# Kernel optimization log

Hardware: AMD Instinct MI355X
Metric: run time of the kernel (lower is better)

## Reference

```python
import jax, jax.numpy as jnp
import numpy as np

B, D, L, TABLE, C, HID = 32768, 8, 16, 524288, 2, 512
GROWTH = 1.3
_PRIMES = [2654436881, 5915587277, 1500450271, 3267000013, 5754853343, 4093082899, 9576890767, 3628273133]
# torch mixes int64/int32 with python-int scalars; only the low 32 bits matter for
# mod-by-power-of-two table_size, so int32 wraparound arithmetic is bit-exact here.
PRIMES32 = jnp.asarray(np.array([p % (1 << 32) for p in _PRIMES], dtype=np.uint64).astype(np.uint32).view(np.int32))


def _linear_init(key, out_f, in_f):
    s = 1.0 / np.sqrt(in_f)
    kw, kb = jax.random.split(key)
    w = jax.random.uniform(kw, (out_f, in_f), jnp.float32, -s, s)
    b = jax.random.uniform(kb, (out_f,), jnp.float32, -s, s)
    return w, b


def setup_inputs() -> dict:
    key = jax.random.key(0)
    ks = jax.random.split(key, 6)
    x = jax.random.normal(ks[0], (B, D), jnp.float32)
    T = jax.random.normal(ks[1], (L, TABLE, C), jnp.float32)
    K = jnp.power(jnp.float32(GROWTH), jnp.arange(L, dtype=jnp.float32))[:, None]  # [L,1]
    l1_w, l1_b = _linear_init(ks[2], HID, D + L * C)
    l2_w, l2_b = _linear_init(ks[3], HID, HID)
    act_w, act_b = _linear_init(ks[4], 4, HID)
    val_w, val_b = _linear_init(ks[5], 1, HID)
    return dict(x=x, T=T, K=K, l1_w=l1_w, l1_b=l1_b, l2_w=l2_w, l2_b=l2_b,
                act_w=act_w, act_b=act_b, val_w=val_w, val_b=val_b)


def reference(x, T, K, l1_w, l1_b, l2_w, l2_b, act_w, act_b, val_w, val_b):
    Bn, Dn = x.shape
    Ln, table_size, Cn = T.shape
    p = jnp.cumsum(x, -1)[:, None, :] * K                      # [B,L,D]
    frac = p - jnp.trunc(p)                                    # torch.frac semantics (sign of p)
    c = jnp.sort(frac, -1)                                     # [B,L,D]
    R = (frac[..., None] >= c[..., None, :]).astype(x.dtype)   # [B,L,D,D]
    R = jnp.concatenate([R, jnp.zeros(R.shape[:-1] + (1,), x.dtype)], -1)  # [B,L,D,D+1]
    c = jnp.concatenate([c, jnp.ones(c.shape[:-1] + (1,), x.dtype)], -1)   # [B,L,D+1]
    A = R + jnp.floor(p)[..., None]                            # [B,L,D,D+1]
    A = A - jnp.concatenate([jnp.zeros_like(A[..., :1, :]), A[..., :-1, :]], -2)
    c = c - jnp.concatenate([jnp.zeros_like(c[..., :1]), c[..., :-1]], -1)
    Ai = A.astype(jnp.int32)                                   # trunc toward zero, like .int()
    terms = Ai * PRIMES32[None, None, :Dn, None]               # int32 wraparound multiply
    cidx = terms[:, :, 0]
    for i in range(1, Dn):                                     # small fixed D, XOR chain
        cidx = jnp.bitwise_xor(cidx, terms[:, :, i])           # [B,L,D+1]
    idx = jnp.mod(cidx, table_size)                            # floor-mod -> non-negative
    f = T[jnp.arange(Ln)[None, :, None], idx]                  # gather -> [B,L,D+1,C]
    f = (f * c[..., None] / K[:, :, None]).sum(2)              # [B,L,C]
    h = jnp.concatenate([x, f.reshape(Bn, -1)], -1)            # [B, D + L*C]
    h = jax.nn.relu(h @ l1_w.T + l1_b)
    h = jax.nn.relu(h @ l2_w.T + l2_b)
    action = h @ act_w.T + act_b                               # [B,4]
    value = h @ val_w.T + val_b                                # [B,1]
    return action, value
```

## Files before the change

### kernel.cpp

```cpp
#include <hip/hip_runtime.h>
#include <cstdint>
#include <cstddef>

#define BB   32768
#define DD   8
#define LLV  16
#define TBL  524288
#define HID  512

typedef __attribute__((ext_vector_type(8))) short short8;
typedef __attribute__((ext_vector_type(8))) unsigned short u16x8;
typedef __attribute__((ext_vector_type(4))) float f32x4;
typedef __attribute__((ext_vector_type(2))) float f32x2;

__device__ __constant__ uint32_t PR[8] = {
    2654436881u, 1620619981u, 1500450271u, 3267000013u,
    1459886047u, 4093082899u,  986956175u, 3628273133u
};

__device__ __forceinline__ unsigned short f2bf(float f) {
    uint32_t u = __float_as_uint(f);
    uint32_t r = (u + 0x7fffu + ((u >> 16) & 1u)) >> 16;
    return (unsigned short)r;
}

__device__ __forceinline__ void gload_lds16(const void* gsrc, void* ldst) {
    __builtin_amdgcn_global_load_lds(
        (const __attribute__((address_space(1))) unsigned int*)gsrc,
        (__attribute__((address_space(3))) unsigned int*)ldst,
        16, 0, 0);
}

__device__ __forceinline__ void enc_idx(const float xs[8], float Kl,
                                        uint32_t idx9[9], float w9[9])
{
    float fr[8];
    int   base[8];
    float cs = 0.f;
#pragma unroll
    for (int i2 = 0; i2 < 8; i2++) {
        cs += xs[i2];
        float p = cs * Kl;
        fr[i2]   = p - truncf(p);
        base[i2] = (int)floorf(p);
    }

    float c[8];
#pragma unroll
    for (int i2 = 0; i2 < 8; i2++) c[i2] = fr[i2];
#define CE(a_, b_) { float lo_ = fminf(c[a_], c[b_]); float hi_ = fmaxf(c[a_], c[b_]); c[a_] = lo_; c[b_] = hi_; }
    CE(0,1) CE(2,3) CE(4,5) CE(6,7)
    CE(0,2) CE(1,3) CE(4,6) CE(5,7)
    CE(1,2) CE(5,6) CE(0,4) CE(3,7)
    CE(1,5) CE(2,6)
    CE(1,4) CE(3,6)
    CE(2,4) CE(3,5)
    CE(3,4)
#undef CE

    float prevc = 0.f;
#pragma unroll
    for (int j = 0; j < 9; j++) {
        float cj = (j < 8) ? c[j] : 1.0f;
        uint32_t h = 0;
        int prev = 0;
#pragma unroll
        for (int i2 = 0; i2 < 8; i2++) {
            int ai = base[i2] + (fr[i2] >= cj ? 1 : 0);
            h ^= (uint32_t)(ai - prev) * PR[i2];
            prev = ai;
        }
        idx9[j] = h & (TBL - 1);
        w9[j]   = cj - prevc;
        prevc   = cj;
    }
}

__global__ __launch_bounds__(256) void k_encode(
    const float* __restrict__ x, const float* __restrict__ T,
    const float* __restrict__ Karr, unsigned short* __restrict__ h0T)
{
    int i = blockIdx.x;
    int l = (i & 7) + ((i >> 10) << 3);
    int b = ((i & 1023) >> 3) * 256 + threadIdx.x;

    const float4 x0 = *(const float4*)(x + (size_t)b * DD);
    const float4 x1 = *(const float4*)(x + (size_t)b * DD + 4);
    float xs[8] = {x0.x, x0.y, x0.z, x0.w, x1.x, x1.y, x1.z, x1.w};

    float Kl = Karr[l];
    const f32x2* Tl = (const f32x2*)(T + ((size_t)l * TBL) * 2);

    uint32_t idx9[9];
    float    w9[9];
    enc_idx(xs, Kl, idx9, w9);

    f32x2 t0, t1, t2, t3, t4, t5, t6, t7, t8;
#define GL(n) asm volatile("global_load_dwordx2 %0, %1, off" \
                           : "=v"(t##n) : "v"(Tl + idx9[n]));
    GL(0) GL(1) GL(2) GL(3) GL(4) GL(5) GL(6) GL(7) GL(8)
#undef GL
    asm volatile("s_waitcnt vmcnt(0)"
        : "+v"(t0), "+v"(t1), "+v"(t2), "+v"(t3), "+v"(t4),
          "+v"(t5), "+v"(t6), "+v"(t7), "+v"(t8));
    __builtin_amdgcn_sched_barrier(0);

    float f0, f1;
    f0 = t0[0] * w9[0];  f1 = t0[1] * w9[0];
    f0 = fmaf(t1[0], w9[1], f0); f1 = fmaf(t1[1], w9[1], f1);
    f0 = fmaf(t2[0], w9[2], f0); f1 = fmaf(t2[1], w9[2], f1);
    f0 = fmaf(t3[0], w9[3], f0); f1 = fmaf(t3[1], w9[3], f1);
    f0 = fmaf(t4[0], w9[4], f0); f1 = fmaf(t4[1], w9[4], f1);
    f0 = fmaf(t5[0], w9[5], f0); f1 = fmaf(t5[1], w9[5], f1);
    f0 = fmaf(t6[0], w9[6], f0); f1 = fmaf(t6[1], w9[6], f1);
    f0 = fmaf(t7[0], w9[7], f0); f1 = fmaf(t7[1], w9[7], f1);
    f0 = fmaf(t8[0], w9[8], f0); f1 = fmaf(t8[1], w9[8], f1);
    f0 /= Kl;
    f1 /= Kl;

    h0T[(size_t)(l * 2 + 0) * BB + b] = f2bf(f0);
    h0T[(size_t)(l * 2 + 1) * BB + b] = f2bf(f1);
}

__global__ __launch_bounds__(256) void k_pack(
    const unsigned short* __restrict__ h0T, const float* __restrict__ x,
    unsigned short* __restrict__ h0b)
{
    int b = blockIdx.x * 256 + threadIdx.x;
    unsigned short row[64];
    const float4 x0 = *(const float4*)(x + (size_t)b * 8);
    const float4 x1 = *(const float4*)(x + (size_t)b * 8 + 4);
    row[0] = f2bf(x0.x); row[1] = f2bf(x0.y); row[2] = f2bf(x0.z); row[3] = f2bf(x0.w);
    row[4] = f2bf(x1.x); row[5] = f2bf(x1.y); row[6] = f2bf(x1.z); row[7] = f2bf(x1.w);
#pragma unroll
    for (int p = 0; p < 32; p++) row[8 + p] = h0T[(size_t)p * BB + b];
#pragma unroll
    for (int c = 40; c < 64; c++) row[c] = 0;
#pragma unroll
    for (int i = 0; i < 8; i++)
        *(u16x8*)(h0b + (size_t)b * 64 + i * 8) = *(u16x8*)(row + i * 8);
}

__global__ __launch_bounds__(256) void k_cvtw(
    const float* __restrict__ w2, unsigned short* __restrict__ w2p,
    const float* __restrict__ w1, unsigned short* __restrict__ w1p)
{
    int bid = blockIdx.x;
    if (bid < 128) {
        int u  = bid * 256 + threadIdx.x;
        int kg = u & 3, kc = (u >> 2) & 15, c = u >> 6;
        const float* src = w2 + (size_t)c * 512 + kc * 32 + kg * 8;
        unsigned short fr[8];
#pragma unroll
        for (int e = 0; e < 8; ++e) fr[e] = f2bf(src[e]);
        *(u16x8*)(w2p + ((((size_t)kc * 512 + c) * 4 + kg) << 3)) = *(u16x8*)fr;
    } else {
        int u  = (bid - 128) * 256 + threadIdx.x;
        int kg = u & 3, ks = (u >> 2) & 1, c = u >> 3;
        int kbase = ks * 32 + kg * 8;
        unsigned short fr[8];
#pragma unroll
        for (int e = 0; e < 8; ++e) {
            int k = kbase + e;
            fr[e] = (k < 40) ? f2bf(w1[(size_t)c * 40 + k]) : (unsigned short)0;
        }
        *(u16x8*)(w1p + ((((size_t)ks * 512 + c) * 4 + kg) << 3)) = *(u16x8*)fr;
    }
}

__global__ __launch_bounds__(512, 2) void k_fused(
    const unsigned short* __restrict__ h0b, const unsigned short* __restrict__ w1p,
    const unsigned short* __restrict__ w2p, const float* __restrict__ b1,
    const float* __restrict__ b2, const float* __restrict__ aw,
    const float* __restrict__ vw, float* __restrict__ hpart)
{
    __shared__ unsigned short h1s[128 * 512];
    __shared__ unsigned short h0s[128 * 64];

    const int tid  = threadIdx.x;
    const int wid  = tid >> 6;
    const int lane = tid & 63;
    const int wm = wid >> 2, wn = wid & 3;
    const int lr = lane & 15;
    const int kg = lane >> 4;
    const int b0 = blockIdx.x * 128;

#pragma unroll
    for (int it = 0; it < 2; ++it) {
        int offb  = (it * 512 + tid) << 4;
        int loffb = offb ^ (((offb >> 7) & 7) << 4);
        int row = loffb >> 7;
        int kel = (loffb & 127) >> 1;
        int ldsbyte = ((it * 512) + (wid * 64)) << 4;
        gload_lds16(h0b + (size_t)(b0 + row) * 64 + kel, (char*)h0s + ldsbyte);
    }
    __syncthreads();

    f32x4 acc[4][8];
#pragma unroll
    for (int m = 0; m < 4; ++m)
#pragma unroll
        for (int n = 0; n < 8; ++n) acc[m][n] = (f32x4){0.f, 0.f, 0.f, 0.f};

#pragma unroll
    for (int ks = 0; ks < 2; ++ks) {
        int kbyte = ks * 64 + kg * 16;
        short8 af[4];
#pragma unroll
        for (int m = 0; m < 4; ++m) {
            int row = wm * 64 + m * 16 + lr;
            int a = ((row << 7) + kbyte) ^ ((row & 7) << 4);
            af[m] = *(const short8*)((const char*)h0s + a);
        }
        short8 bfr[8];
#pragma unroll
        for (int n = 0; n < 8; ++n) {
            int col = wn * 128 + n * 16 + lr;
            bfr[n] = *(const short8*)(w1p + ((((size_t)ks * 512 + col) * 4 + kg) << 3));
        }
#pragma unroll
        for (int m = 0; m < 4; ++m)
#pragma unroll
            for (int n = 0; n < 8; ++n)
                acc[m][n] = __builtin_amdgcn_mfma_f32_16x16x32_bf16(
                    af[m], bfr[n], acc[m][n], 0, 0, 0);
    }

#pragma unroll
    for (int n = 0; n < 8; ++n) {
        int col = wn * 128 + n * 16 + lr;
        float b1v = b1[col];
#pragma unroll
        for (int m = 0; m < 4; ++m) {
#pragma unroll
            for (int r = 0; r < 4; ++r) {
                int row = wm * 64 + m * 16 + kg * 4 + r;
                int byte = ((row << 10) + col * 2) ^ ((row & 7) << 4);
                *(unsigned short*)((char*)h1s + byte) =
                    f2bf(fmaxf(acc[m][n][r] + b1v, 0.f));
            }
        }
    }
    __syncthreads();

#pragma unroll
    for (int m = 0; m < 4; ++m)
#pragma unroll
        for (int n = 0; n < 8; ++n) acc[m][n] = (f32x4){0.f, 0.f, 0.f, 0.f};

    short8 aX[4], bX[8], aY[4], bY[8];

#define LDA(dst, kc)                                                            \
    _Pragma("unroll")                                                           \
    for (int m = 0; m < 4; ++m) {                                               \
        int row = wm * 64 + m * 16 + lr;                                        \
        int a = (((row << 10) + (kc) * 64 + kg * 16)) ^ ((row & 7) << 4);       \
        dst[m] = *(const short8*)((const char*)h1s + a);                        \
    }
#define LDB(dst, kc)                                                            \
    _Pragma("unroll")                                                           \
    for (int n = 0; n < 8; ++n) {                                               \
        int col = wn * 128 + n * 16 + lr;                                       \
        dst[n] = *(const short8*)(w2p + ((((size_t)(kc) * 512 + col) * 4 + kg) << 3)); \
    }
#define MM(aa, bb)                                                              \
    __builtin_amdgcn_sched_barrier(0);                                          \
    __builtin_amdgcn_s_setprio(1);                                              \
    _Pragma("unroll")                                                           \
    for (int m = 0; m < 4; ++m)                                                 \
        _Pragma("unroll")                                                       \
        for (int n = 0; n < 8; ++n)                                             \
            acc[m][n] = __builtin_amdgcn_mfma_f32_16x16x32_bf16(                \
                aa[m], bb[n], acc[m][n], 0, 0, 0);                              \
    __builtin_amdgcn_s_setprio(0);

    LDA(aX, 0)  LDB(bX, 0)
    LDA(aY, 1)  LDB(bY, 1)  MM(aX, bX)
    LDA(aX, 2)  LDB(bX, 2)  MM(aY, bY)
    LDA(aY, 3)  LDB(bY, 3)  MM(aX, bX)
    LDA(aX, 4)  LDB(bX, 4)  MM(aY, bY)
    LDA(aY, 5)  LDB(bY, 5)  MM(aX, bX)
    LDA(aX, 6)  LDB(bX, 6)  MM(aY, bY)
    LDA(aY, 7)  LDB(bY, 7)  MM(aX, bX)
    LDA(aX, 8)  LDB(bX, 8)  MM(aY, bY)
    LDA(aY, 9)  LDB(bY, 9)  MM(aX, bX)
    LDA(aX, 10) LDB(bX, 10) MM(aY, bY)
    LDA(aY, 11) LDB(bY, 11) MM(aX, bX)
    LDA(aX, 12) LDB(bX, 12) MM(aY, bY)
    LDA(aY, 13) LDB(bY, 13) MM(aX, bX)
    LDA(aX, 14) LDB(bX, 14) MM(aY, bY)
    LDA(aY, 15) LDB(bY, 15) MM(aX, bX)
    MM(aY, bY)
#undef LDA
#undef LDB
#undef MM

#pragma unroll
    for (int n = 0; n < 8; ++n) {
        int col = wn * 128 + n * 16 + lr;
        float b2v = b2[col];
#pragma unroll
        for (int m = 0; m < 4; ++m)
#pragma unroll
            for (int r = 0; r < 4; ++r)
                acc[m][n][r] = fmaxf(acc[m][n][r] + b2v, 0.f);
    }

    float hwv[5][8];
#pragma unroll
    for (int n = 0; n < 8; ++n) {
        int col = wn * 128 + n * 16 + lr;
        hwv[0][n] = aw[col];
        hwv[1][n] = aw[512 + col];
        hwv[2][n] = aw[1024 + col];
        hwv[3][n] = aw[1536 + col];
        hwv[4][n] = vw[col];
    }
    float* hp = hpart + (size_t)wn * (BB * 5);
#pragma unroll
    for (int hm = 0; hm < 5; ++hm) {
        f32x4 p[4];
#pragma unroll
        for (int m = 0; m < 4; ++m) {
            p[m] = acc[m][0] * hwv[hm][0];
#pragma unroll
            for (int n = 1; n < 8; ++n) p[m] += acc[m][n] * hwv[hm][n];
        }
#pragma unroll
        for (int d = 1; d < 16; d <<= 1)
#pragma unroll
            for (int m = 0; m < 4; ++m)
#pragma unroll
                for (int r = 0; r < 4; ++r)
                    p[m][r] += __shfl_xor(p[m][r], d);
        if (lr == 0) {
#pragma unroll
            for (int m = 0; m < 4; ++m)
#pragma unroll
                for (int r = 0; r < 4; ++r)
                    hp[(size_t)(b0 + wm * 64 + m * 16 + kg * 4 + r) * 5 + hm] = p[m][r];
        }
    }
}

__global__ __launch_bounds__(256) void k_hreduce(
    const float* __restrict__ hpart, const float* __restrict__ ab,
    const float* __restrict__ vb, float* __restrict__ out)
{
    int i = blockIdx.x * 256 + threadIdx.x;
    int b = i / 5;
    int hm = i - b * 5;
    float s = 0.f;
#pragma unroll
    for (int g = 0; g < 4; ++g) s += hpart[(size_t)g * (BB * 5) + i];
    s += (hm < 4) ? ab[hm] : vb[0];
    if (hm < 4) out[(size_t)b * 4 + hm] = s;
    else        out[(size_t)BB * 4 + b] = s;
}

extern "C" void kernel_launch(void* const* d_in, const int* in_sizes, int n_in,
                              void* d_out, int out_size, void* d_ws, size_t ws_size,
                              hipStream_t stream)
{
    const float* x    = (const float*)d_in[0];
    const float* T    = (const float*)d_in[1];
    const float* K    = (const float*)d_in[2];
    const float* l1w  = (const float*)d_in[3];
    const float* l1b  = (const float*)d_in[4];
    const float* l2w  = (const float*)d_in[5];
    const float* l2b  = (const float*)d_in[6];
    const float* actw = (const float*)d_in[7];
    const float* actb = (const float*)d_in[8];
    const float* valw = (const float*)d_in[9];
    const float* valb = (const float*)d_in[10];
    float* out = (float*)d_out;

    char* ws = (char*)d_ws;
    unsigned short* h0b   = (unsigned short*)ws;
    unsigned short* h0T   = (unsigned short*)(ws + 4194304);
    unsigned short* w2p   = (unsigned short*)(ws + 6291456);
    unsigned short* w1p   = (unsigned short*)(ws + 6815744);
    float*          hpart = (float*)(ws + 6881280);

    k_encode  <<<2048, 256, 0, stream>>>(x, T, K, h0T);
    k_cvtw    <<<144, 256, 0, stream>>>(l2w, w2p, l1w, w1p);
    k_pack    <<<BB / 256, 256, 0, stream>>>(h0T, x, h0b);
    k_fused   <<<256, 512, 0, stream>>>(h0b, w1p, w2p, l1b, l2b, actw, valw, hpart);
    k_hreduce <<<BB * 5 / 256, 256, 0, stream>>>(hpart, actb, valb, out);
}
```

Measured before the change: 68.43 us.

## Fuse pack and head-reduce kernels into the fused MLP kernel

Removes the separate pack kernel by having the fused MLP kernel read the transposed encoding and x directly into swizzled shared memory, zero-padding the unused columns. It also removes the head-reduce kernel by reducing the four per-wave-column partials in shared memory and writing action and value outputs with their biases directly. This saves two launches and the global round trips through the h0b and hpart buffers. In exchange it uses scalar 2-byte LDS stores with possible bank conflicts instead of async global-to-LDS loads, and adds an extra block barrier.

```diff
diff --git a/kernel.cpp b/kernel.cpp
--- a/kernel.cpp
+++ b/kernel.cpp
@@ -22,13 +22,6 @@
     uint32_t u = __float_as_uint(f);
     uint32_t r = (u + 0x7fffu + ((u >> 16) & 1u)) >> 16;
     return (unsigned short)r;
-}
-
-__device__ __forceinline__ void gload_lds16(const void* gsrc, void* ldst) {
-    __builtin_amdgcn_global_load_lds(
-        (const __attribute__((address_space(1))) unsigned int*)gsrc,
-        (__attribute__((address_space(3))) unsigned int*)ldst,
-        16, 0, 0);
 }
 
 __device__ __forceinline__ void enc_idx(const float xs[8], float Kl,
@@ -122,25 +115,6 @@
     h0T[(size_t)(l * 2 + 1) * BB + b] = f2bf(f1);
 }
 
-__global__ __launch_bounds__(256) void k_pack(
-    const unsigned short* __restrict__ h0T, const float* __restrict__ x,
-    unsigned short* __restrict__ h0b)
-{
-    int b = blockIdx.x * 256 + threadIdx.x;
-    unsigned short row[64];
-    const float4 x0 = *(const float4*)(x + (size_t)b * 8);
-    const float4 x1 = *(const float4*)(x + (size_t)b * 8 + 4);
-    row[0] = f2bf(x0.x); row[1] = f2bf(x0.y); row[2] = f2bf(x0.z); row[3] = f2bf(x0.w);
-    row[4] = f2bf(x1.x); row[5] = f2bf(x1.y); row[6] = f2bf(x1.z); row[7] = f2bf(x1.w);
-#pragma unroll
-    for (int p = 0; p < 32; p++) row[8 + p] = h0T[(size_t)p * BB + b];
-#pragma unroll
-    for (int c = 40; c < 64; c++) row[c] = 0;
-#pragma unroll
-    for (int i = 0; i < 8; i++)
-        *(u16x8*)(h0b + (size_t)b * 64 + i * 8) = *(u16x8*)(row + i * 8);
-}
-
 __global__ __launch_bounds__(256) void k_cvtw(
     const float* __restrict__ w2, unsigned short* __restrict__ w2p,
     const float* __restrict__ w1, unsigned short* __restrict__ w1p)
@@ -169,10 +143,12 @@
 }
 
 __global__ __launch_bounds__(512, 2) void k_fused(
-    const unsigned short* __restrict__ h0b, const unsigned short* __restrict__ w1p,
-    const unsigned short* __restrict__ w2p, const float* __restrict__ b1,
-    const float* __restrict__ b2, const float* __restrict__ aw,
-    const float* __restrict__ vw, float* __restrict__ hpart)
+    const unsigned short* __restrict__ h0T, const float* __restrict__ x,
+    const unsigned short* __restrict__ w1p, const unsigned short* __restrict__ w2p,
+    const float* __restrict__ b1, const float* __restrict__ b2,
+    const float* __restrict__ aw, const float* __restrict__ ab,
+    const float* __restrict__ vw, const float* __restrict__ vb,
+    float* __restrict__ out)
 {
     __shared__ unsigned short h1s[128 * 512];
     __shared__ unsigned short h0s[128 * 64];
@@ -185,14 +161,30 @@
     const int kg = lane >> 4;
     const int b0 = blockIdx.x * 128;
 
-#pragma unroll
-    for (int it = 0; it < 2; ++it) {
-        int offb  = (it * 512 + tid) << 4;
-        int loffb = offb ^ (((offb >> 7) & 7) << 4);
-        int row = loffb >> 7;
-        int kel = (loffb & 127) >> 1;
-        int ldsbyte = ((it * 512) + (wid * 64)) << 4;
-        gload_lds16(h0b + (size_t)(b0 + row) * 64 + kel, (char*)h0s + ldsbyte);
+    {
+        int p = tid >> 4, c = tid & 15;
+        u16x8 v = *(const u16x8*)(h0T + (size_t)p * BB + b0 + c * 8);
+#pragma unroll
+        for (int e = 0; e < 8; ++e) {
+            int row = c * 8 + e;
+            int byte = ((row << 7) + (8 + p) * 2) ^ ((row & 7) << 4);
+            *(unsigned short*)((char*)h0s + byte) = v[e];
+        }
+        if (tid < 128) {
+            int row = tid;
+            const float4 x0 = *(const float4*)(x + (size_t)(b0 + row) * 8);
+            const float4 x1 = *(const float4*)(x + (size_t)(b0 + row) * 8 + 4);
+            unsigned short xv[8] = {
+                f2bf(x0.x), f2bf(x0.y), f2bf(x0.z), f2bf(x0.w),
+                f2bf(x1.x), f2bf(x1.y), f2bf(x1.z), f2bf(x1.w)};
+            *(u16x8*)((char*)h0s + ((row << 7) ^ ((row & 7) << 4))) = *(u16x8*)xv;
+        } else {
+            int t2 = tid - 128;
+            int row = t2 / 3, seg = t2 - row * 3;
+            int byte = ((row << 7) + 80 + seg * 16) ^ ((row & 7) << 4);
+            u16x8 z = {0, 0, 0, 0, 0, 0, 0, 0};
+            *(u16x8*)((char*)h0s + byte) = z;
+        }
     }
     __syncthreads();
 
@@ -316,7 +308,7 @@
         hwv[3][n] = aw[1536 + col];
         hwv[4][n] = vw[col];
     }
-    float* hp = hpart + (size_t)wn * (BB * 5);
+    float* spart = (float*)h0s;
 #pragma unroll
     for (int hm = 0; hm < 5; ++hm) {
         f32x4 p[4];
@@ -338,24 +330,24 @@
             for (int m = 0; m < 4; ++m)
 #pragma unroll
                 for (int r = 0; r < 4; ++r)
-                    hp[(size_t)(b0 + wm * 64 + m * 16 + kg * 4 + r) * 5 + hm] = p[m][r];
-        }
-    }
-}
-
-__global__ __launch_bounds__(256) void k_hreduce(
-    const float* __restrict__ hpart, const float* __restrict__ ab,
-    const float* __restrict__ vb, float* __restrict__ out)
-{
-    int i = blockIdx.x * 256 + threadIdx.x;
-    int b = i / 5;
-    int hm = i - b * 5;
-    float s = 0.f;
-#pragma unroll
-    for (int g = 0; g < 4; ++g) s += hpart[(size_t)g * (BB * 5) + i];
-    s += (hm < 4) ? ab[hm] : vb[0];
-    if (hm < 4) out[(size_t)b * 4 + hm] = s;
-    else        out[(size_t)BB * 4 + b] = s;
+                    spart[(wn * 5 + hm) * 128 + wm * 64 + m * 16 + kg * 4 + r] = p[m][r];
+        }
+    }
+    __syncthreads();
+
+    if (tid < 128) {
+        int b = b0 + tid;
+        float s[5];
+#pragma unroll
+        for (int hm = 0; hm < 5; ++hm) {
+            float v = spart[(0 * 5 + hm) * 128 + tid] + spart[(1 * 5 + hm) * 128 + tid]
+                    + spart[(2 * 5 + hm) * 128 + tid] + spart[(3 * 5 + hm) * 128 + tid];
+            s[hm] = v;
+        }
+        float4 act = make_float4(s[0] + ab[0], s[1] + ab[1], s[2] + ab[2], s[3] + ab[3]);
+        *(float4*)(out + (size_t)b * 4) = act;
+        out[(size_t)BB * 4 + b] = s[4] + vb[0];
+    }
 }
 
 extern "C" void kernel_launch(void* const* d_in, const int* in_sizes, int n_in,
@@ -376,15 +368,12 @@
     float* out = (float*)d_out;
 
     char* ws = (char*)d_ws;
-    unsigned short* h0b   = (unsigned short*)ws;
-    unsigned short* h0T   = (unsigned short*)(ws + 4194304);
-    unsigned short* w2p   = (unsigned short*)(ws + 6291456);
-    unsigned short* w1p   = (unsigned short*)(ws + 6815744);
-    float*          hpart = (float*)(ws + 6881280);
-
-    k_encode  <<<2048, 256, 0, stream>>>(x, T, K, h0T);
-    k_cvtw    <<<144, 256, 0, stream>>>(l2w, w2p, l1w, w1p);
-    k_pack    <<<BB / 256, 256, 0, stream>>>(h0T, x, h0b);
-    k_fused   <<<256, 512, 0, stream>>>(h0b, w1p, w2p, l1b, l2b, actw, valw, hpart);
-    k_hreduce <<<BB * 5 / 256, 256, 0, stream>>>(hpart, actb, valb, out);
-}
+    unsigned short* h0T = (unsigned short*)ws;
+    unsigned short* w2p = (unsigned short*)(ws + 2097152);
+    unsigned short* w1p = (unsigned short*)(ws + 2621440);
+
+    k_encode <<<2048, 256, 0, stream>>>(x, T, K, h0T);
+    k_cvtw   <<<144, 256, 0, stream>>>(l2w, w2p, l1w, w1p);
+    k_fused  <<<256, 512, 0, stream>>>(h0T, x, w1p, w2p, l1b, l2b,
+                                       actw, actb, valw, valb, out);
+}
```

Result: faster. 61.90 us (-9.5%).
